# Performance work log

Hardware: AMD Instinct MI355X
Metric: run time of the kernel (lower is better)

The kernel has to match this reference:

```python
import jax, jax.numpy as jnp
import numpy as np

LAMBDA_DRO = 0.1
EPSILON = 0.5
EPS = 1e-8

N, M, D, K = 2048, 4096, 512, 1000


def _cosine_matrix(a, b):
    # a: [N, d], b: [M, d] -> [N, M] cosine similarity via normalize + GEMM
    an = a / jnp.maximum(jnp.linalg.norm(a, axis=1, keepdims=True), EPS)
    bn = b / jnp.maximum(jnp.linalg.norm(b, axis=1, keepdims=True), EPS)
    return an @ bn.T


def setup_inputs() -> dict:
    key = jax.random.key(0)
    k = jax.random.split(key, 7)
    return {
        "ptr_features": jax.random.normal(k[0], (N, D), dtype=jnp.float32),
        "ptr_logits": jax.random.normal(k[1], (N, K), dtype=jnp.float32),
        "ptr_labels": jax.random.randint(k[2], (N,), 0, K),
        "nu_features": jax.random.normal(k[3], (M, D), dtype=jnp.float32),
        "nu_logits": jax.random.normal(k[4], (M, K), dtype=jnp.float32),
        "nu_labels": jax.random.randint(k[5], (M,), 0, K),
        "classifier_weights": jax.random.normal(k[6], (K, D), dtype=jnp.float32),
    }


def reference(ptr_features, ptr_logits, ptr_labels, nu_features, nu_logits,
              nu_labels, classifier_weights):
    # per-sample CE loss on nu (hard labels)
    log_probs = jax.nn.log_softmax(nu_logits, axis=1)          # [M, K]
    nu_losses = -jnp.take_along_axis(log_probs, nu_labels[:, None], axis=1)[:, 0]  # [M]

    # transport costs
    C_X = 1.0 - _cosine_matrix(ptr_features, nu_features)       # [N, M]
    ptr_emb = classifier_weights[ptr_labels]                    # [N, d]
    nu_emb = classifier_weights[nu_labels]                      # [M, d]
    C_Y = 1.0 - _cosine_matrix(ptr_emb, nu_emb)                 # [N, M]
    C_total = C_X + C_Y

    # worst-case distribution Q^lambda
    exponent = (nu_losses[None, :] - LAMBDA_DRO * C_total) / (LAMBDA_DRO * EPSILON + EPS)
    exponent = exponent - jnp.max(exponent, axis=1, keepdims=True)
    exp_terms = jnp.exp(exponent)                               # [N, M]
    weights = exp_terms / (jnp.sum(exp_terms, axis=1, keepdims=True) + EPS)
    probs = jnp.mean(weights, axis=0)                           # [M]
    probs = probs / (jnp.sum(probs) + EPS)

    dro_loss = jnp.sum(probs * nu_losses)
    total_loss = dro_loss  # semantic_loss = 0 (no moco inputs)
    return (total_loss, dro_loss, probs, jnp.mean(C_total), jnp.mean(C_X), jnp.mean(C_Y))
```

## Files before the change

kernel.cpp:

```cpp
#include <hip/hip_runtime.h>
#include <math.h>

#define N_PTR 2048
#define M_NU  4096
#define DIM   512
#define KCLS  1000
#define KPAD  1024

static constexpr float LAMBDA_ = 0.1f;
static constexpr float EPS_ = 1e-8f;
static constexpr float INV_DENOM = 1.0f / (0.1f * 0.5f + 1e-8f);

typedef short short8 __attribute__((ext_vector_type(8)));
typedef unsigned short u16x8 __attribute__((ext_vector_type(8)));
typedef float f32x4 __attribute__((ext_vector_type(4)));

__device__ __forceinline__ unsigned short f2bf(float x) {
  unsigned u = __float_as_uint(x);
  u += 0x7fff + ((u >> 16) & 1);
  return (unsigned short)(u >> 16);
}
__device__ __forceinline__ float bf2f(unsigned short h) {
  return __uint_as_float(((unsigned)h) << 16);
}

__device__ __forceinline__ void gload16(const void* g, void* l) {
  __builtin_amdgcn_global_load_lds(
      (const __attribute__((address_space(1))) unsigned int*)g,
      (__attribute__((address_space(3))) unsigned int*)l, 16, 0, 0);
}

__device__ __forceinline__ float blk_reduce_sum(float v, float* red) {
  #pragma unroll
  for (int off = 32; off > 0; off >>= 1) v += __shfl_down(v, off);
  __syncthreads();
  if ((threadIdx.x & 63) == 0) red[threadIdx.x >> 6] = v;
  __syncthreads();
  return red[0] + red[1] + red[2] + red[3];
}

__device__ __forceinline__ float blk_reduce_max(float v, float* red) {
  #pragma unroll
  for (int off = 32; off > 0; off >>= 1) v = fmaxf(v, __shfl_down(v, off));
  __syncthreads();
  if ((threadIdx.x & 63) == 0) red[threadIdx.x >> 6] = v;
  __syncthreads();
  return fmaxf(fmaxf(red[0], red[1]), fmaxf(red[2], red[3]));
}

__device__ __forceinline__ float blk512_reduce_sum(float v, float* red) {
  #pragma unroll
  for (int off = 32; off > 0; off >>= 1) v += __shfl_down(v, off);
  __syncthreads();
  if ((threadIdx.x & 63) == 0) red[threadIdx.x >> 6] = v;
  __syncthreads();
  float s = 0.f;
  #pragma unroll
  for (int i = 0; i < 8; ++i) s += red[i];
  return s;
}

__global__ __launch_bounds__(256) void prep_kernel(
    const float* __restrict__ ptr_f, const float* __restrict__ nu_f,
    const float* __restrict__ cls_f, const float* __restrict__ logits,
    const int* __restrict__ labels, unsigned short* __restrict__ An,
    unsigned short* __restrict__ Bn, unsigned short* __restrict__ Cn,
    float* __restrict__ losses) {
  __shared__ float red[4];
  int b = blockIdx.x;
  if (b < 1792) {
    int gid = b * 256 + threadIdx.x;
    int row = gid >> 6, lane = gid & 63;
    const float* src; unsigned short* dst; int lrow; int in_rows;
    if (row < N_PTR)             { src = ptr_f; dst = An; lrow = row;                in_rows = N_PTR; }
    else if (row < N_PTR + M_NU) { src = nu_f;  dst = Bn; lrow = row - N_PTR;        in_rows = M_NU; }
    else                         { src = cls_f; dst = Cn; lrow = row - N_PTR - M_NU; in_rows = KCLS; }
    u16x8 ov;
    if (lrow < in_rows) {
      const float4* rp = (const float4*)(src + (size_t)lrow * DIM);
      float4 a = rp[lane * 2], bq = rp[lane * 2 + 1];
      float v[8] = {a.x, a.y, a.z, a.w, bq.x, bq.y, bq.z, bq.w};
      float s = 0.f;
      #pragma unroll
      for (int j = 0; j < 8; ++j) s = fmaf(v[j], v[j], s);
      #pragma unroll
      for (int off = 32; off > 0; off >>= 1) s += __shfl_xor(s, off);
      float inv = 1.0f / fmaxf(sqrtf(s), EPS_);
      #pragma unroll
      for (int j = 0; j < 8; ++j) ov[j] = f2bf(v[j] * inv);
    } else {
      #pragma unroll
      for (int j = 0; j < 8; ++j) ov[j] = 0;
    }
    *(u16x8*)(dst + (size_t)lrow * DIM + lane * 8) = ov;
  } else {
    int row = b - 1792;
    int tid = threadIdx.x;
    const float* x = logits + (size_t)row * KCLS;
    const float4* x4 = (const float4*)x;
    float4 v = make_float4(0.f, 0.f, 0.f, 0.f);
    float mx_loc = -INFINITY;
    if (tid < 250) {
      v = x4[tid];
      mx_loc = fmaxf(fmaxf(v.x, v.y), fmaxf(v.z, v.w));
    }
    float mx = blk_reduce_max(mx_loc, red);
    float se_loc = 0.f;
    if (tid < 250)
      se_loc = __expf(v.x - mx) + __expf(v.y - mx) + __expf(v.z - mx) + __expf(v.w - mx);
    float se = blk_reduce_sum(se_loc, red);
    if (tid == 0) losses[row] = mx + logf(se) - x[labels[row]];
  }
}

template <int BM, int MODE>
__global__ __launch_bounds__(256) void mfma_gemm(
    const unsigned short* __restrict__ A, const unsigned short* __restrict__ B,
    unsigned short* __restrict__ Gfb, unsigned short* __restrict__ Tb,
    const int* __restrict__ pl, const int* __restrict__ nl,
    const float* __restrict__ nu_loss, unsigned* __restrict__ gbits,
    float* __restrict__ pr, float* __restrict__ pr2,
    float* __restrict__ s_part, float* __restrict__ gy_part, int ldc) {
  constexpr int FR = BM / 32;
  constexpr int WSPAN = BM / 2;
  __shared__ unsigned short Alds[BM * 64];
  __shared__ unsigned short Blds[BM * 64];
  __shared__ float red[4];
  const int tid = threadIdx.x;
  const int w = tid >> 6, lane = tid & 63;
  const int brow = blockIdx.y * BM, bcol = blockIdx.x * BM;
  const int wr = w >> 1, wc = w & 1;

  if (MODE == 0 && blockIdx.x == 0 && blockIdx.y == 0) {
    float mloc = 0.f;
    for (int i = tid; i < M_NU; i += 256) mloc = fmaxf(mloc, nu_loss[i]);
    float mx = blk_reduce_max(mloc, red);
    if (tid == 0) *gbits = __float_as_uint(mx);
    __syncthreads();
  }

  const int sr = lane >> 3;
  const int sc = lane & 7;
  const int schunk = (sc ^ sr) * 8;

  f32x4 acc[FR][FR] = {};

  for (int k0 = 0; k0 < DIM; k0 += 64) {
    #pragma unroll
    for (int i = 0; i < FR; ++i) {
      int j = w * FR + i;
      int r = j * 8 + sr;
      gload16(A + (size_t)(brow + r) * DIM + k0 + schunk, (char*)Alds + j * 1024);
      gload16(B + (size_t)(bcol + r) * DIM + k0 + schunk, (char*)Blds + j * 1024);
    }
    __syncthreads();
    #pragma unroll
    for (int kk = 0; kk < 2; ++kk) {
      const int koff = kk * 64 + (lane >> 4) * 16;
      short8 af[FR], bfr[FR];
      #pragma unroll
      for (int mi = 0; mi < FR; ++mi) {
        int r = wr * WSPAN + mi * 16 + (lane & 15);
        af[mi] = *(const short8*)((const char*)Alds + r * 128 + (koff ^ ((r & 7) << 4)));
      }
      #pragma unroll
      for (int ni = 0; ni < FR; ++ni) {
        int r = wc * WSPAN + ni * 16 + (lane & 15);
        bfr[ni] = *(const short8*)((const char*)Blds + r * 128 + (koff ^ ((r & 7) << 4)));
      }
      #pragma unroll
      for (int mi = 0; mi < FR; ++mi)
        #pragma unroll
        for (int ni = 0; ni < FR; ++ni)
          acc[mi][ni] = __builtin_amdgcn_mfma_f32_16x16x32_bf16(af[mi], bfr[ni], acc[mi][ni], 0, 0, 0);
    }
    __syncthreads();
  }

  if (MODE == 0) {
    #pragma unroll
    for (int mi = 0; mi < FR; ++mi)
      #pragma unroll
      for (int ni = 0; ni < FR; ++ni)
        #pragma unroll
        for (int j = 0; j < 4; ++j) {
          int row = brow + wr * WSPAN + mi * 16 + (lane >> 4) * 4 + j;
          int col = bcol + wc * WSPAN + ni * 16 + (lane & 15);
          Gfb[(size_t)row * ldc + col] = f2bf(acc[mi][ni][j]);
        }
  }
}

__global__ __launch_bounds__(512, 4) void sgemm8_kernel(
    const unsigned short* __restrict__ A, const unsigned short* __restrict__ B,
    const unsigned short* __restrict__ Gfb, unsigned short* __restrict__ Tb,
    const int* __restrict__ pl, const int* __restrict__ nl,
    const float* __restrict__ nu_loss, const unsigned* __restrict__ gbits,
    float* __restrict__ pr, float* __restrict__ pr2,
    float* __restrict__ s_part, float* __restrict__ gy_part) {
  __shared__ unsigned short Alds[128 * 64];
  __shared__ unsigned short Blds[128 * 64];
  __shared__ float red[8];
  const int tid = threadIdx.x;
  const int w = tid >> 6, lane = tid & 63;
  const int brow = blockIdx.y * 128, bcol = blockIdx.x * 128;
  const int wr = w >> 2, wc = w & 3;

  const int sr = lane >> 3;
  const int sc = lane & 7;
  const int schunk = (sc ^ sr) * 8;

  f32x4 acc[4][2] = {};

  for (int k0 = 0; k0 < DIM; k0 += 64) {
    #pragma unroll
    for (int i = 0; i < 2; ++i) {
      int j = w * 2 + i;
      int r = j * 8 + sr;
      gload16(A + (size_t)(brow + r) * DIM + k0 + schunk, (char*)Alds + j * 1024);
      gload16(B + (size_t)(bcol + r) * DIM + k0 + schunk, (char*)Blds + j * 1024);
    }
    __syncthreads();
    #pragma unroll
    for (int kk = 0; kk < 2; ++kk) {
      const int koff = kk * 64 + (lane >> 4) * 16;
      short8 af[4], bfr[2];
      #pragma unroll
      for (int mi = 0; mi < 4; ++mi) {
        int r = wr * 64 + mi * 16 + (lane & 15);
        af[mi] = *(const short8*)((const char*)Alds + r * 128 + (koff ^ ((r & 7) << 4)));
      }
      #pragma unroll
      for (int ni = 0; ni < 2; ++ni) {
        int r = wc * 32 + ni * 16 + (lane & 15);
        bfr[ni] = *(const short8*)((const char*)Blds + r * 128 + (koff ^ ((r & 7) << 4)));
      }
      #pragma unroll
      for (int mi = 0; mi < 4; ++mi)
        #pragma unroll
        for (int ni = 0; ni < 2; ++ni)
          acc[mi][ni] = __builtin_amdgcn_mfma_f32_16x16x32_bf16(af[mi], bfr[ni], acc[mi][ni], 0, 0, 0);
    }
    __syncthreads();
  }

  const float gmax = __uint_as_float(*gbits);
  const float fac = LAMBDA_ * INV_DENOM;
  int cols[2]; float a_r[2]; float loss_r[2]; int nl_r[2];
  #pragma unroll
  for (int ni = 0; ni < 2; ++ni) {
    cols[ni]   = bcol + wc * 32 + ni * 16 + (lane & 15);
    loss_r[ni] = nu_loss[cols[ni]];
    a_r[ni]    = (loss_r[ni] - gmax - 2.f * LAMBDA_) * INV_DENOM;
    nl_r[ni]   = nl[cols[ni]];
  }
  float s_acc = 0.f, gy_acc = 0.f;
  #pragma unroll
  for (int mi = 0; mi < 4; ++mi) {
    #pragma unroll
    for (int j = 0; j < 4; ++j) {
      int row = brow + wr * 64 + mi * 16 + (lane >> 4) * 4 + j;
      const unsigned short* Grow = Gfb + (size_t)pl[row] * KPAD;
      float rowacc = 0.f, rowacc2 = 0.f;
      #pragma unroll
      for (int ni = 0; ni < 2; ++ni) {
        float s  = acc[mi][ni][j];
        float gy = bf2f(Grow[nl_r[ni]]);
        float e  = fmaf(fac, s + gy, a_r[ni]);
        float t  = __expf(e);
        unsigned short tb = f2bf(t);
        Tb[(size_t)row * M_NU + cols[ni]] = tb;
        float tt = bf2f(tb);
        rowacc  += tt;
        rowacc2 += tt * loss_r[ni];
        s_acc += s; gy_acc += gy;
      }
      #pragma unroll
      for (int off = 1; off < 16; off <<= 1) {
        rowacc  += __shfl_xor(rowacc, off);
        rowacc2 += __shfl_xor(rowacc2, off);
      }
      if ((lane & 15) == 0) {
        pr [(size_t)(blockIdx.x * 4 + wc) * N_PTR + row] = rowacc;
        pr2[(size_t)(blockIdx.x * 4 + wc) * N_PTR + row] = rowacc2;
      }
    }
  }
  float stot = blk512_reduce_sum(s_acc, red);
  float gtot = blk512_reduce_sum(gy_acc, red);
  if (tid == 0) {
    int bid = blockIdx.y * gridDim.x + blockIdx.x;
    s_part[bid] = stot; gy_part[bid] = gtot;
  }
}

__global__ __launch_bounds__(256) void colpass_td_kernel(
    const unsigned short* __restrict__ Tb, const float* __restrict__ pr,
    const float* __restrict__ pr2, float* __restrict__ partial,
    float* __restrict__ T_part, float* __restrict__ D_part) {
  __shared__ float sh[64];
  int b = blockIdx.x, tid = threadIdx.x;
  if (b < 256) {
    int bx = b & 7, by = b >> 3;
    int m0 = bx * 512 + tid * 2;
    int n0 = by * 64;
    if (tid < 64) {
      float rs = 0.f;
      #pragma unroll 4
      for (int cb = 0; cb < 128; ++cb) rs += pr[(size_t)cb * N_PTR + n0 + tid];
      sh[tid] = 1.0f / (rs + EPS_);
    }
    __syncthreads();
    float a0 = 0.f, a1 = 0.f;
    #pragma unroll 4
    for (int i = 0; i < 64; ++i) {
      unsigned tv = *(const unsigned*)(Tb + (size_t)(n0 + i) * M_NU + m0);
      float wv = sh[i];
      a0 = fmaf(bf2f((unsigned short)(tv & 0xffffu)), wv, a0);
      a1 = fmaf(bf2f((unsigned short)(tv >> 16)), wv, a1);
    }
    *(float2*)(partial + (size_t)by * M_NU + m0) = make_float2(a0, a1);
  } else {
    int n = (b - 256) * 128 + (tid & 127);
    float tl = 0.f, dl = 0.f;
    if (tid < 128) {
      float rs = 0.f, wl = 0.f;
      #pragma unroll 4
      for (int cb = 0; cb < 128; ++cb) {
        rs += pr [(size_t)cb * N_PTR + n];
        wl += pr2[(size_t)cb * N_PTR + n];
      }
      float wi = 1.0f / (rs + EPS_);
      tl = rs * wi; dl = wl * wi;
    }
    __syncthreads();
    #pragma unroll
    for (int off = 32; off > 0; off >>= 1) { tl += __shfl_down(tl, off); dl += __shfl_down(dl, off); }
    if ((tid & 63) == 0) { sh[tid >> 6] = tl; sh[4 + (tid >> 6)] = dl; }
    __syncthreads();
    if (tid == 0) {
      T_part[b - 256] = sh[0] + sh[1] + sh[2] + sh[3];
      D_part[b - 256] = sh[4] + sh[5] + sh[6] + sh[7];
    }
  }
}

__global__ __launch_bounds__(256) void final_kernel(const float* __restrict__ partial,
    const float* __restrict__ T_part, const float* __restrict__ D_part,
    const float* __restrict__ s_part, const float* __restrict__ gy_part,
    float* __restrict__ out) {
  __shared__ float red[4];
  int b = blockIdx.x, tid = threadIdx.x;
  float T = 0.f;
  #pragma unroll
  for (int i = 0; i < 16; ++i) T += T_part[i];
  float scale = (1.0f / (float)N_PTR) / (T / (float)N_PTR + EPS_);
  if (b < 16) {
    int m = b * 256 + tid;
    float raw = 0.f;
    #pragma unroll
    for (int c = 0; c < 32; ++c) raw += partial[(size_t)c * M_NU + m];
    out[2 + m] = raw * scale;
  } else {
    float D = 0.f;
    #pragma unroll
    for (int i = 0; i < 16; ++i) D += D_part[i];
    float ls = 0.f, lg = 0.f;
    for (int i = tid; i < 512; i += 256) { ls += s_part[i]; lg += gy_part[i]; }
    float S  = blk_reduce_sum(ls, red);
    float Gy = blk_reduce_sum(lg, red);
    if (tid == 0) {
      float dro = D * scale;
      const float invNM = 1.0f / ((float)N_PTR * (float)M_NU);
      float mcx = 1.f - S * invNM;
      float mcy = 1.f - Gy * invNM;
      out[0] = dro;
      out[1] = dro;
      out[2 + M_NU] = mcx + mcy;
      out[3 + M_NU] = mcx;
      out[4 + M_NU] = mcy;
    }
  }
}

extern "C" void kernel_launch(void* const* d_in, const int* in_sizes, int n_in,
                              void* d_out, int out_size, void* d_ws, size_t ws_size,
                              hipStream_t stream) {
  const float* ptr_feat = (const float*)d_in[0];
  const int*   ptr_lab  = (const int*)d_in[2];
  const float* nu_feat  = (const float*)d_in[3];
  const float* nu_log   = (const float*)d_in[4];
  const int*   nu_lab   = (const int*)d_in[5];
  const float* cls_w    = (const float*)d_in[6];
  float* out = (float*)d_out;

  char* base = (char*)d_ws;
  unsigned short* Tb  = (unsigned short*)base;
  unsigned short* Gfb = (unsigned short*)(base + 16u * 1024 * 1024);
  unsigned short* An  = (unsigned short*)(base + 18u * 1024 * 1024);
  unsigned short* Bn  = (unsigned short*)(base + 20u * 1024 * 1024);
  unsigned short* Cn  = (unsigned short*)(base + 24u * 1024 * 1024);
  float* fb           = (float*)(base + 25u * 1024 * 1024);
  float* nloss   = fb;
  unsigned* gbits= (unsigned*)(nloss + 4096);
  float* pr      = nloss + 4096 + 64;
  float* pr2     = pr  + 128 * N_PTR;
  float* partial = pr2 + 128 * N_PTR;
  float* s_part  = partial + 32 * M_NU;
  float* gy_part = s_part + 512;
  float* T_part  = gy_part + 512;
  float* D_part  = T_part + 16;

  prep_kernel<<<dim3(1792 + M_NU), 256, 0, stream>>>(
      ptr_feat, nu_feat, cls_w, nu_log, nu_lab, An, Bn, Cn, nloss);
  mfma_gemm<64, 0><<<dim3(KPAD / 64, KPAD / 64), 256, 0, stream>>>(
      Cn, Cn, Gfb, nullptr, nullptr, nullptr, nloss, gbits,
      nullptr, nullptr, nullptr, nullptr, KPAD);
  sgemm8_kernel<<<dim3(M_NU / 128, N_PTR / 128), 512, 0, stream>>>(
      An, Bn, Gfb, Tb, ptr_lab, nu_lab, nloss, gbits,
      pr, pr2, s_part, gy_part);
  colpass_td_kernel<<<dim3(272), 256, 0, stream>>>(Tb, pr, pr2, partial, T_part, D_part);
  final_kernel<<<dim3(17), 256, 0, stream>>>(partial, T_part, D_part, s_part, gy_part, out);
}
```

Baseline: 66.33 us.

## Use 4-wave 64x64 warp tiles and stage gathered label-cosine tile in LDS

The main GEMM kernel moves from 8 waves with 64x32 warp tiles to 4 waves with 64x64 warp tiles. This gives more MFMA work per fragment load and halves the per-row partial sums, so the column pass now reads 64 partials per row instead of 128. The gathered classifier-cosine values for the 128x128 tile are prefetched into LDS during the k-loop instead of being fetched as scattered global loads in the epilogue. The cost is more registers and LDS per block, which can lower occupancy.

Result: slower. 76.54 us (+15.4%).

```diff
diff --git a/kernel.cpp b/kernel.cpp
--- a/kernel.cpp
+++ b/kernel.cpp
@@ -46,18 +46,6 @@
   if ((threadIdx.x & 63) == 0) red[threadIdx.x >> 6] = v;
   __syncthreads();
   return fmaxf(fmaxf(red[0], red[1]), fmaxf(red[2], red[3]));
-}
-
-__device__ __forceinline__ float blk512_reduce_sum(float v, float* red) {
-  #pragma unroll
-  for (int off = 32; off > 0; off >>= 1) v += __shfl_down(v, off);
-  __syncthreads();
-  if ((threadIdx.x & 63) == 0) red[threadIdx.x >> 6] = v;
-  __syncthreads();
-  float s = 0.f;
-  #pragma unroll
-  for (int i = 0; i < 8; ++i) s += red[i];
-  return s;
 }
 
 __global__ __launch_bounds__(256) void prep_kernel(
@@ -191,7 +179,7 @@
   }
 }
 
-__global__ __launch_bounds__(512, 4) void sgemm8_kernel(
+__global__ __launch_bounds__(256) void sgemm_kernel(
     const unsigned short* __restrict__ A, const unsigned short* __restrict__ B,
     const unsigned short* __restrict__ Gfb, unsigned short* __restrict__ Tb,
     const int* __restrict__ pl, const int* __restrict__ nl,
@@ -200,22 +188,41 @@
     float* __restrict__ s_part, float* __restrict__ gy_part) {
   __shared__ unsigned short Alds[128 * 64];
   __shared__ unsigned short Blds[128 * 64];
-  __shared__ float red[8];
+  __shared__ unsigned short Gt[128][136];
+  __shared__ int pll[128];
+  __shared__ int nll[128];
+  __shared__ float red[4];
   const int tid = threadIdx.x;
   const int w = tid >> 6, lane = tid & 63;
   const int brow = blockIdx.y * 128, bcol = blockIdx.x * 128;
-  const int wr = w >> 2, wc = w & 3;
+  const int wr = w >> 1, wc = w & 1;
+
+  if (tid < 128) pll[tid] = pl[brow + tid];
+  else           nll[tid - 128] = nl[bcol + tid - 128];
+  __syncthreads();
 
   const int sr = lane >> 3;
   const int sc = lane & 7;
   const int schunk = (sc ^ sr) * 8;
 
-  f32x4 acc[4][2] = {};
-
-  for (int k0 = 0; k0 < DIM; k0 += 64) {
-    #pragma unroll
-    for (int i = 0; i < 2; ++i) {
-      int j = w * 2 + i;
+  const int gr = tid >> 4;
+  const int gc0 = (tid & 15) * 8;
+
+  f32x4 acc[4][4] = {};
+
+  #pragma unroll
+  for (int kt = 0; kt < 8; ++kt) {
+    const int k0 = kt * 64;
+    {
+      int r = kt * 16 + gr;
+      const unsigned short* grow = Gfb + (size_t)pll[r] * KPAD;
+      #pragma unroll
+      for (int cc = 0; cc < 8; ++cc)
+        Gt[r][gc0 + cc] = grow[nll[gc0 + cc]];
+    }
+    #pragma unroll
+    for (int i = 0; i < 4; ++i) {
+      int j = w * 4 + i;
       int r = j * 8 + sr;
       gload16(A + (size_t)(brow + r) * DIM + k0 + schunk, (char*)Alds + j * 1024);
       gload16(B + (size_t)(bcol + r) * DIM + k0 + schunk, (char*)Blds + j * 1024);
@@ -224,21 +231,21 @@
     #pragma unroll
     for (int kk = 0; kk < 2; ++kk) {
       const int koff = kk * 64 + (lane >> 4) * 16;
-      short8 af[4], bfr[2];
+      short8 af[4], bfr[4];
       #pragma unroll
       for (int mi = 0; mi < 4; ++mi) {
         int r = wr * 64 + mi * 16 + (lane & 15);
         af[mi] = *(const short8*)((const char*)Alds + r * 128 + (koff ^ ((r & 7) << 4)));
       }
       #pragma unroll
-      for (int ni = 0; ni < 2; ++ni) {
-        int r = wc * 32 + ni * 16 + (lane & 15);
+      for (int ni = 0; ni < 4; ++ni) {
+        int r = wc * 64 + ni * 16 + (lane & 15);
         bfr[ni] = *(const short8*)((const char*)Blds + r * 128 + (koff ^ ((r & 7) << 4)));
       }
       #pragma unroll
       for (int mi = 0; mi < 4; ++mi)
         #pragma unroll
-        for (int ni = 0; ni < 2; ++ni)
+        for (int ni = 0; ni < 4; ++ni)
           acc[mi][ni] = __builtin_amdgcn_mfma_f32_16x16x32_bf16(af[mi], bfr[ni], acc[mi][ni], 0, 0, 0);
     }
     __syncthreads();
@@ -246,26 +253,26 @@
 
   const float gmax = __uint_as_float(*gbits);
   const float fac = LAMBDA_ * INV_DENOM;
-  int cols[2]; float a_r[2]; float loss_r[2]; int nl_r[2];
-  #pragma unroll
-  for (int ni = 0; ni < 2; ++ni) {
-    cols[ni]   = bcol + wc * 32 + ni * 16 + (lane & 15);
+  int cols[4]; int cloc[4]; float a_r[4]; float loss_r[4];
+  #pragma unroll
+  for (int ni = 0; ni < 4; ++ni) {
+    cloc[ni]   = wc * 64 + ni * 16 + (lane & 15);
+    cols[ni]   = bcol + cloc[ni];
     loss_r[ni] = nu_loss[cols[ni]];
     a_r[ni]    = (loss_r[ni] - gmax - 2.f * LAMBDA_) * INV_DENOM;
-    nl_r[ni]   = nl[cols[ni]];
   }
   float s_acc = 0.f, gy_acc = 0.f;
   #pragma unroll
   for (int mi = 0; mi < 4; ++mi) {
     #pragma unroll
     for (int j = 0; j < 4; ++j) {
-      int row = brow + wr * 64 + mi * 16 + (lane >> 4) * 4 + j;
-      const unsigned short* Grow = Gfb + (size_t)pl[row] * KPAD;
+      int rloc = wr * 64 + mi * 16 + (lane >> 4) * 4 + j;
+      int row = brow + rloc;
       float rowacc = 0.f, rowacc2 = 0.f;
       #pragma unroll
-      for (int ni = 0; ni < 2; ++ni) {
+      for (int ni = 0; ni < 4; ++ni) {
         float s  = acc[mi][ni][j];
-        float gy = bf2f(Grow[nl_r[ni]]);
+        float gy = bf2f(Gt[rloc][cloc[ni]]);
         float e  = fmaf(fac, s + gy, a_r[ni]);
         float t  = __expf(e);
         unsigned short tb = f2bf(t);
@@ -281,13 +288,13 @@
         rowacc2 += __shfl_xor(rowacc2, off);
       }
       if ((lane & 15) == 0) {
-        pr [(size_t)(blockIdx.x * 4 + wc) * N_PTR + row] = rowacc;
-        pr2[(size_t)(blockIdx.x * 4 + wc) * N_PTR + row] = rowacc2;
-      }
-    }
-  }
-  float stot = blk512_reduce_sum(s_acc, red);
-  float gtot = blk512_reduce_sum(gy_acc, red);
+        pr [(size_t)(blockIdx.x * 2 + wc) * N_PTR + row] = rowacc;
+        pr2[(size_t)(blockIdx.x * 2 + wc) * N_PTR + row] = rowacc2;
+      }
+    }
+  }
+  float stot = blk_reduce_sum(s_acc, red);
+  float gtot = blk_reduce_sum(gy_acc, red);
   if (tid == 0) {
     int bid = blockIdx.y * gridDim.x + blockIdx.x;
     s_part[bid] = stot; gy_part[bid] = gtot;
@@ -307,7 +314,7 @@
     if (tid < 64) {
       float rs = 0.f;
       #pragma unroll 4
-      for (int cb = 0; cb < 128; ++cb) rs += pr[(size_t)cb * N_PTR + n0 + tid];
+      for (int cb = 0; cb < 64; ++cb) rs += pr[(size_t)cb * N_PTR + n0 + tid];
       sh[tid] = 1.0f / (rs + EPS_);
     }
     __syncthreads();
@@ -326,7 +333,7 @@
     if (tid < 128) {
       float rs = 0.f, wl = 0.f;
       #pragma unroll 4
-      for (int cb = 0; cb < 128; ++cb) {
+      for (int cb = 0; cb < 64; ++cb) {
         rs += pr [(size_t)cb * N_PTR + n];
         wl += pr2[(size_t)cb * N_PTR + n];
       }
@@ -404,8 +411,8 @@
   float* nloss   = fb;
   unsigned* gbits= (unsigned*)(nloss + 4096);
   float* pr      = nloss + 4096 + 64;
-  float* pr2     = pr  + 128 * N_PTR;
-  float* partial = pr2 + 128 * N_PTR;
+  float* pr2     = pr  + 64 * N_PTR;
+  float* partial = pr2 + 64 * N_PTR;
   float* s_part  = partial + 32 * M_NU;
   float* gy_part = s_part + 512;
   float* T_part  = gy_part + 512;
@@ -416,7 +423,7 @@
   mfma_gemm<64, 0><<<dim3(KPAD / 64, KPAD / 64), 256, 0, stream>>>(
       Cn, Cn, Gfb, nullptr, nullptr, nullptr, nloss, gbits,
       nullptr, nullptr, nullptr, nullptr, KPAD);
-  sgemm8_kernel<<<dim3(M_NU / 128, N_PTR / 128), 512, 0, stream>>>(
+  sgemm_kernel<<<dim3(M_NU / 128, N_PTR / 128), 256, 0, stream>>>(
       An, Bn, Gfb, Tb, ptr_lab, nu_lab, nloss, gbits,
       pr, pr2, s_part, gy_part);
   colpass_td_kernel<<<dim3(272), 256, 0, stream>>>(Tb, pr, pr2, partial, T_part, D_part);
```
